# Kernel tuning notes

Measured on AMD Instinct MI355X. Metric: run time of the kernel, lower is better.

The kernel has to match this reference:

```python
import jax, jax.numpy as jnp
import numpy as np

N_NODES = 50000
N_PAIRS = 800000
F = 128


def setup_inputs() -> dict:
    key = jax.random.key(0)
    ks = jax.random.split(key, 6)
    x = jax.random.normal(ks[0], (N_NODES, F), dtype=jnp.float32)
    w_ij = jax.random.normal(ks[1], (N_PAIRS, F), dtype=jnp.float32)
    # Lecun-normal-ish init for Dense layers (flax default scale)
    W1 = jax.random.normal(ks[2], (3 * F, F), dtype=jnp.float32) / np.sqrt(3 * F)
    b1 = jnp.zeros((F,), dtype=jnp.float32)
    W2 = jax.random.normal(ks[3], (F, 1), dtype=jnp.float32) / np.sqrt(F)
    b2 = jnp.zeros((1,), dtype=jnp.float32)
    idx_i = jax.random.randint(ks[4], (N_PAIRS,), 0, N_NODES)
    idx_j = jax.random.randint(ks[5], (N_PAIRS,), 0, N_NODES)
    return {"x": x, "w_ij": w_ij, "W1": W1, "b1": b1, "W2": W2, "b2": b2,
            "idx_i": idx_i, "idx_j": idx_j}


def reference(x, w_ij, W1, b1, W2, b2, idx_i, idx_j):
    # gather node embeddings for each pair
    q_i = x[idx_i]                      # (n_pairs, F)
    k_j = x[idx_j]                      # (n_pairs, F)
    y = jnp.concatenate([q_i, k_j, w_ij], axis=-1)   # (n_pairs, 3F)
    # 2-layer MLP: Dense(F) -> silu -> Dense(1)
    h = jax.nn.silu(y @ W1 + b1)        # (n_pairs, F)
    out = (h @ W2 + b2).squeeze(axis=-1)  # (n_pairs,)
    return out
```

## Files before the change

kernel.cpp:

```cpp
#include <hip/hip_runtime.h>

constexpr int FD = 128;
constexpr int NNODES = 50000;
constexpr int NPAIRS = 800000;

typedef _Float16 half8 __attribute__((ext_vector_type(8)));
typedef __fp16 fp16x2 __attribute__((ext_vector_type(2)));
typedef float f32x4 __attribute__((ext_vector_type(4)));

#define MFMA16(a, b, c) __builtin_amdgcn_mfma_f32_16x16x32_f16((a), (b), (c), 0, 0, 0)

__device__ __forceinline__ void cvt_hilo2(float a, float b, unsigned& hi, unsigned& lo) {
    fp16x2 h = __builtin_amdgcn_cvt_pkrtz(a, b);
    float ra = a - (float)h[0];
    float rb = b - (float)h[1];
    fp16x2 l = __builtin_amdgcn_cvt_pkrtz(ra, rb);
    hi = __builtin_bit_cast(unsigned, h);
    lo = __builtin_bit_cast(unsigned, l);
}

__device__ __forceinline__ void cvt_hilo8(const float* s, half8& hi, half8& lo) {
    union { half8 v; unsigned u[4]; } uh, ul;
    cvt_hilo2(s[0], s[1], uh.u[0], ul.u[0]);
    cvt_hilo2(s[2], s[3], uh.u[1], ul.u[1]);
    cvt_hilo2(s[4], s[5], uh.u[2], ul.u[2]);
    cvt_hilo2(s[6], s[7], uh.u[3], ul.u[3]);
    hi = uh.v; lo = ul.v;
}

__device__ __forceinline__ int swz(int row, int col) {
    return row * FD + (col ^ ((row & 7) << 3));
}

__device__ __forceinline__ void load_w1_frags(const float* __restrict__ W1, int arow0,
                                              int r, int g, int wave,
                                              half8 Ahi[2][4], half8 Alo[2][4]) {
#pragma unroll
    for (int nt = 0; nt < 2; ++nt) {
        int n = (wave * 2 + nt) * 16 + r;
#pragma unroll
        for (int ks = 0; ks < 4; ++ks) {
            float s[8];
#pragma unroll
            for (int j = 0; j < 8; ++j)
                s[j] = W1[(arow0 + ks * 32 + g * 8 + j) * FD + n];
            cvt_hilo8(s, Ahi[nt][ks], Alo[nt][ks]);
        }
    }
}

__global__ __launch_bounds__(256, 2) void node_kernel(
    const float* __restrict__ x, const float* __restrict__ W1,
    float* __restrict__ xab)
{
    __shared__ __align__(16) _Float16 sHi[64 * FD];
    __shared__ __align__(16) _Float16 sLo[64 * FD];

    const int tid = threadIdx.x;
    const int lane = tid & 63, wave = tid >> 6;
    const int r = lane & 15, g = lane >> 4;
    const int h = blockIdx.y;

    half8 Ahi[2][4], Alo[2][4];
    load_w1_frags(W1, h * FD, r, g, wave, Ahi, Alo);

    const int m0 = blockIdx.x * 64;
    const f32x4* xv = reinterpret_cast<const f32x4*>(x);
#pragma unroll
    for (int rr = 0; rr < 8; ++rr) {
        int v = tid + 256 * rr;
        int row = v >> 5, c4 = v & 31;
        int srow = m0 + row; if (srow >= NNODES) srow = NNODES - 1;
        f32x4 d = xv[(size_t)srow * 32 + c4];
        unsigned h0, l0, h1, l1;
        cvt_hilo2(d[0], d[1], h0, l0);
        cvt_hilo2(d[2], d[3], h1, l1);
        int sidx = swz(row, c4 * 4);
        *reinterpret_cast<uint2*>(&sHi[sidx]) = make_uint2(h0, h1);
        *reinterpret_cast<uint2*>(&sLo[sidx]) = make_uint2(l0, l1);
    }
    __syncthreads();

    f32x4 acc[2][4] = {};
#pragma unroll
    for (int ks = 0; ks < 4; ++ks) {
#pragma unroll
        for (int mt = 0; mt < 4; ++mt) {
            int ridx = swz(mt * 16 + r, ks * 32 + g * 8);
            half8 bh = *reinterpret_cast<const half8*>(&sHi[ridx]);
            half8 bl = *reinterpret_cast<const half8*>(&sLo[ridx]);
#pragma unroll
            for (int nt = 0; nt < 2; ++nt) {
                acc[nt][mt] = MFMA16(Ahi[nt][ks], bh, acc[nt][mt]);
                acc[nt][mt] = MFMA16(Alo[nt][ks], bh, acc[nt][mt]);
                acc[nt][mt] = MFMA16(Ahi[nt][ks], bl, acc[nt][mt]);
            }
        }
    }

#pragma unroll
    for (int mt = 0; mt < 4; ++mt) {
        int node = m0 + mt * 16 + r;
        if (node < NNODES) {
#pragma unroll
            for (int nt = 0; nt < 2; ++nt) {
                int nc = h * FD + (wave * 2 + nt) * 16 + g * 4;
                *reinterpret_cast<f32x4*>(&xab[(size_t)node * 256 + nc]) = acc[nt][mt];
            }
        }
    }
}

__global__ __launch_bounds__(256, 2) void pair_kernel(
    const float* __restrict__ wij, const float* __restrict__ W1,
    const float* __restrict__ b1, const float* __restrict__ W2,
    const float* __restrict__ b2, const int* __restrict__ idx_i,
    const int* __restrict__ idx_j, const float* __restrict__ xab,
    float* __restrict__ out)
{
    __shared__ __align__(16) _Float16 sHi[64 * FD];
    __shared__ __align__(16) _Float16 sLo[64 * FD];
    __shared__ float sred[4][64];

    const int tid = threadIdx.x;
    const int lane = tid & 63, wave = tid >> 6;
    const int r = lane & 15, g = lane >> 4;

    half8 Ahi[2][4], Alo[2][4];
    load_w1_frags(W1, 2 * FD, r, g, wave, Ahi, Alo);

    f32x4 b1v[2], w2v[2];
#pragma unroll
    for (int nt = 0; nt < 2; ++nt) {
        int nc = (wave * 2 + nt) * 16 + g * 4;
        b1v[nt] = *reinterpret_cast<const f32x4*>(&b1[nc]);
        w2v[nt] = *reinterpret_cast<const f32x4*>(&W2[nc]);
    }
    const float b2v = b2[0];

    for (int t = blockIdx.x; t < NPAIRS / 64; t += gridDim.x) {
        const int m0 = t * 64;
        const f32x4* wrow = reinterpret_cast<const f32x4*>(wij + (size_t)m0 * FD);
#pragma unroll
        for (int rr = 0; rr < 8; ++rr) {
            int v = tid + 256 * rr;
            int row = v >> 5, c4 = v & 31;
            f32x4 d = wrow[v];
            unsigned h0, l0, h1, l1;
            cvt_hilo2(d[0], d[1], h0, l0);
            cvt_hilo2(d[2], d[3], h1, l1);
            int sidx = swz(row, c4 * 4);
            *reinterpret_cast<uint2*>(&sHi[sidx]) = make_uint2(h0, h1);
            *reinterpret_cast<uint2*>(&sLo[sidx]) = make_uint2(l0, l1);
        }
        __syncthreads();

        f32x4 acc[2][4] = {};
#pragma unroll
        for (int ks = 0; ks < 4; ++ks) {
#pragma unroll
            for (int mt = 0; mt < 4; ++mt) {
                int ridx = swz(mt * 16 + r, ks * 32 + g * 8);
                half8 bh = *reinterpret_cast<const half8*>(&sHi[ridx]);
                half8 bl = *reinterpret_cast<const half8*>(&sLo[ridx]);
#pragma unroll
                for (int nt = 0; nt < 2; ++nt) {
                    acc[nt][mt] = MFMA16(Ahi[nt][ks], bh, acc[nt][mt]);
                    acc[nt][mt] = MFMA16(Alo[nt][ks], bh, acc[nt][mt]);
                    acc[nt][mt] = MFMA16(Ahi[nt][ks], bl, acc[nt][mt]);
                }
            }
        }

#pragma unroll
        for (int mt = 0; mt < 4; ++mt) {
            int p = m0 + mt * 16 + r;
            int ni = idx_i[p], nj = idx_j[p];
            float ps = 0.f;
#pragma unroll
            for (int nt = 0; nt < 2; ++nt) {
                int nc = (wave * 2 + nt) * 16 + g * 4;
                f32x4 xa = *reinterpret_cast<const f32x4*>(&xab[(size_t)ni * 256 + nc]);
                f32x4 xb = *reinterpret_cast<const f32x4*>(&xab[(size_t)nj * 256 + 128 + nc]);
                f32x4 tv = acc[nt][mt] + b1v[nt] + xa + xb;
#pragma unroll
                for (int e = 0; e < 4; ++e) {
                    float te = tv[e];
                    float hh = te / (1.f + __expf(-te));
                    ps += hh * w2v[nt][e];
                }
            }
            ps += __shfl_xor(ps, 16);
            ps += __shfl_xor(ps, 32);
            if (g == 0) sred[wave][mt * 16 + r] = ps;
        }
        __syncthreads();
        if (wave == 0)
            out[m0 + lane] = b2v + sred[0][lane] + sred[1][lane] + sred[2][lane] + sred[3][lane];
    }
}

extern "C" void kernel_launch(void* const* d_in, const int* in_sizes, int n_in,
                              void* d_out, int out_size, void* d_ws, size_t ws_size,
                              hipStream_t stream) {
    const float* x   = (const float*)d_in[0];
    const float* wij = (const float*)d_in[1];
    const float* W1  = (const float*)d_in[2];
    const float* b1  = (const float*)d_in[3];
    const float* W2  = (const float*)d_in[4];
    const float* b2  = (const float*)d_in[5];
    const int* ii    = (const int*)d_in[6];
    const int* jj    = (const int*)d_in[7];
    float* out = (float*)d_out;
    float* xab = (float*)d_ws;

    dim3 gnode((NNODES + 63) / 64, 2);
    node_kernel<<<gnode, 256, 0, stream>>>(x, W1, xab);
    pair_kernel<<<1024, 256, 0, stream>>>(wij, W1, b1, W2, b2, ii, jj, xab, out);
}
```

Baseline: 804.5 us.

## Prefetch next pair tile and indices into registers during compute

The pair kernel now loads the next tile's w_ij rows and idx_i/idx_j into registers while the current tile's MFMA and epilogue run, then rotates the buffers. Launch bounds go to 3 blocks per CU and the grid shrinks to 768 persistent blocks. This is meant to hide global load latency behind compute. It adds register pressure that could cause spills or limit occupancy.

Result: faster. 757.8 us (-5.8%).

```diff
diff --git a/kernel.cpp b/kernel.cpp
--- a/kernel.cpp
+++ b/kernel.cpp
@@ -111,7 +111,7 @@
     }
 }
 
-__global__ __launch_bounds__(256, 2) void pair_kernel(
+__global__ __launch_bounds__(256, 3) void pair_kernel(
     const float* __restrict__ wij, const float* __restrict__ W1,
     const float* __restrict__ b1, const float* __restrict__ W2,
     const float* __restrict__ b2, const int* __restrict__ idx_i,
@@ -138,22 +138,50 @@
     }
     const float b2v = b2[0];
 
-    for (int t = blockIdx.x; t < NPAIRS / 64; t += gridDim.x) {
-        const int m0 = t * 64;
-        const f32x4* wrow = reinterpret_cast<const f32x4*>(wij + (size_t)m0 * FD);
+    const int ntiles = NPAIRS / 64;
+    const f32x4* wv = reinterpret_cast<const f32x4*>(wij);
+
+    int t = blockIdx.x;
+    f32x4 P[8];
+    int pi[4], pj[4];
+    {
+        const size_t base = (size_t)t * 2048 + tid;
+#pragma unroll
+        for (int rr = 0; rr < 8; ++rr) P[rr] = wv[base + 256 * rr];
+#pragma unroll
+        for (int mt = 0; mt < 4; ++mt) {
+            int p = t * 64 + mt * 16 + r;
+            pi[mt] = idx_i[p]; pj[mt] = idx_j[p];
+        }
+    }
+
+    for (; t < ntiles; t += gridDim.x) {
 #pragma unroll
         for (int rr = 0; rr < 8; ++rr) {
             int v = tid + 256 * rr;
             int row = v >> 5, c4 = v & 31;
-            f32x4 d = wrow[v];
             unsigned h0, l0, h1, l1;
-            cvt_hilo2(d[0], d[1], h0, l0);
-            cvt_hilo2(d[2], d[3], h1, l1);
+            cvt_hilo2(P[rr][0], P[rr][1], h0, l0);
+            cvt_hilo2(P[rr][2], P[rr][3], h1, l1);
             int sidx = swz(row, c4 * 4);
             *reinterpret_cast<uint2*>(&sHi[sidx]) = make_uint2(h0, h1);
             *reinterpret_cast<uint2*>(&sLo[sidx]) = make_uint2(l0, l1);
         }
         __syncthreads();
+
+        const int tn = t + gridDim.x;
+        const bool has_next = tn < ntiles;
+        f32x4 Q[8]; int qi[4], qj[4];
+        if (has_next) {
+            const size_t base = (size_t)tn * 2048 + tid;
+#pragma unroll
+            for (int rr = 0; rr < 8; ++rr) Q[rr] = wv[base + 256 * rr];
+#pragma unroll
+            for (int mt = 0; mt < 4; ++mt) {
+                int p = tn * 64 + mt * 16 + r;
+                qi[mt] = idx_i[p]; qj[mt] = idx_j[p];
+            }
+        }
 
         f32x4 acc[2][4] = {};
 #pragma unroll
@@ -172,10 +200,10 @@
             }
         }
 
+        const int m0 = t * 64;
 #pragma unroll
         for (int mt = 0; mt < 4; ++mt) {
-            int p = m0 + mt * 16 + r;
-            int ni = idx_i[p], nj = idx_j[p];
+            int ni = pi[mt], nj = pj[mt];
             float ps = 0.f;
 #pragma unroll
             for (int nt = 0; nt < 2; ++nt) {
@@ -197,6 +225,13 @@
         __syncthreads();
         if (wave == 0)
             out[m0 + lane] = b2v + sred[0][lane] + sred[1][lane] + sred[2][lane] + sred[3][lane];
+
+        if (has_next) {
+#pragma unroll
+            for (int rr = 0; rr < 8; ++rr) P[rr] = Q[rr];
+#pragma unroll
+            for (int mt = 0; mt < 4; ++mt) { pi[mt] = qi[mt]; pj[mt] = qj[mt]; }
+        }
     }
 }
 
@@ -216,5 +251,5 @@
 
     dim3 gnode((NNODES + 63) / 64, 2);
     node_kernel<<<gnode, 256, 0, stream>>>(x, W1, xab);
-    pair_kernel<<<1024, 256, 0, stream>>>(wij, W1, b1, W2, b2, ii, jj, xab, out);
-}
+    pair_kernel<<<768, 256, 0, stream>>>(wij, W1, b1, W2, b2, ii, jj, xab, out);
+}
```
